# Kernel tuning notes

Hardware: AMD Instinct MI355X
Metric: run time of the kernel (lower is better)

The kernel has to match this reference:

```python
import jax, jax.numpy as jnp
import numpy as np

N_NODES = 20000
N_EDGES = 320000
N_GRAPHS = 64
D = 128  # node_dim


def _gat_conv(h, W, al, ar, b, src, dst, n, res=None, act=None):
    # DGL GATConv: fc -> per-head attn logits -> leaky_relu -> edge softmax per dst -> scatter-add
    H, Dh = al.shape
    feat = (h @ W).reshape(n, H, Dh)                      # [N,H,D]
    el = jnp.einsum('nhd,hd->nh', feat, al)               # [N,H]
    er = jnp.einsum('nhd,hd->nh', feat, ar)               # [N,H]
    e = jax.nn.leaky_relu(el[src] + er[dst], 0.2)         # [E,H]
    m = jax.ops.segment_max(e, dst, num_segments=n)       # [N,H]
    m = jnp.where(jnp.isfinite(m), m, 0.0)
    a = jnp.exp(e - m[dst])                               # [E,H]
    den = jax.ops.segment_sum(a, dst, num_segments=n)     # [N,H]
    a = a / jnp.maximum(den, 1e-9)[dst]
    out = jax.ops.segment_sum(a[:, :, None] * feat[src], dst, num_segments=n)  # [N,H,D]
    if res is not None:
        out = out + res
    out = out + b.reshape(1, H, Dh)
    return act(out) if act is not None else out


def setup_inputs() -> dict:
    key = jax.random.key(0)
    ks = jax.random.split(key, 20)
    s = 0.05
    inp = {
        'h': jax.random.normal(ks[0], (N_NODES, D), jnp.float32),
        'he': jax.random.normal(ks[1], (N_EDGES, 64), jnp.float32),
        'src': jax.random.randint(ks[2], (N_EDGES,), 0, N_NODES),
        'dst': jax.random.randint(ks[3], (N_EDGES,), 0, N_NODES),
        'graph_id': jnp.sort(jax.random.randint(ks[4], (N_NODES,), 0, N_GRAPHS)),
        # layer 0: in=D, heads=4, out=D
        'W0': jax.random.normal(ks[5], (D, 4 * D), jnp.float32) * s,
        'al0': jax.random.normal(ks[6], (4, D), jnp.float32) * s,
        'ar0': jax.random.normal(ks[7], (4, D), jnp.float32) * s,
        'b0': jnp.zeros((4 * D,), jnp.float32),
        # layer 1: in=4D, heads=4, out=D, residual (identity since 4D==4*D)
        'W1': jax.random.normal(ks[8], (4 * D, 4 * D), jnp.float32) * s,
        'al1': jax.random.normal(ks[9], (4, D), jnp.float32) * s,
        'ar1': jax.random.normal(ks[10], (4, D), jnp.float32) * s,
        'b1': jnp.zeros((4 * D,), jnp.float32),
        # layer 2: in=4D, heads=6, out=D, residual via res_fc (4D -> 6D)
        'W2': jax.random.normal(ks[11], (4 * D, 6 * D), jnp.float32) * s,
        'al2': jax.random.normal(ks[12], (6, D), jnp.float32) * s,
        'ar2': jax.random.normal(ks[13], (6, D), jnp.float32) * s,
        'b2': jnp.zeros((6 * D,), jnp.float32),
        'resW2': jax.random.normal(ks[14], (4 * D, 6 * D), jnp.float32) * s,
        # final MLP (1 layer): Linear(D, D)
        'Wm': jax.random.normal(ks[15], (D, D), jnp.float32) * s,
        'bm': jnp.zeros((D,), jnp.float32),
    }
    return inp


def reference(h, he, src, dst, graph_id, W0, al0, ar0, b0, W1, al1, ar1, b1,
              W2, al2, ar2, b2, resW2, Wm, bm):
    n = h.shape[0]
    elu = jax.nn.elu
    # layer 0 (no residual, elu), flatten heads
    x = _gat_conv(h, W0, al0, ar0, b0, src, dst, n, res=None, act=elu)
    x = x.reshape(n, -1)  # [N, 4D]
    # layer 1 (identity residual, elu), flatten heads
    res1 = x.reshape(n, 4, D)
    x2 = _gat_conv(x, W1, al1, ar1, b1, src, dst, n, res=res1, act=elu)
    x2 = x2.reshape(n, -1)  # [N, 4D]
    # layer 2 (linear residual, no activation), mean over heads
    res2 = (x2 @ resW2).reshape(n, 6, D)
    x3 = _gat_conv(x2, W2, al2, ar2, b2, src, dst, n, res=res2, act=None)
    local_feat = x3.mean(axis=1)  # [N, D]
    # avg pooling per graph + linear
    sums = jax.ops.segment_sum(local_feat, graph_id, num_segments=N_GRAPHS)
    cnts = jax.ops.segment_sum(jnp.ones((n,), local_feat.dtype), graph_id, num_segments=N_GRAPHS)
    pooled = sums / jnp.maximum(cnts, 1.0)[:, None]  # [G, D]
    global_feat = pooled @ Wm + bm
    return (local_feat, global_feat)
```

## Files before the change

### kernel.cpp

```cpp
#include <hip/hip_runtime.h>
#include <math.h>


typedef _Float16 f16;
typedef __attribute__((ext_vector_type(8))) _Float16 half8;
typedef __attribute__((ext_vector_type(4))) _Float16 half4;
typedef __attribute__((ext_vector_type(4))) float float4v;

union U16 { unsigned short u; _Float16 h; };

#define M_PAD 20096
#define CHSTRIDE ((size_t)M_PAD * 64)

__device__ inline void gload_lds16(const void* g, void* l) {
    __builtin_amdgcn_global_load_lds((const __attribute__((address_space(1))) unsigned*)g,
                                     (__attribute__((address_space(3))) unsigned*)l,
                                     16, 0, 0);
}


__global__ __launch_bounds__(256) void deg_kernel(const int* __restrict__ dst,
                                                  int* __restrict__ deg, int E) {
    int e = blockIdx.x * 256 + threadIdx.x;
    if (e < E) atomicAdd(&deg[dst[e]], 1);
}

__global__ __launch_bounds__(1024) void scan_kernel(const int* __restrict__ deg,
                                                    int* __restrict__ row_off,
                                                    const int* __restrict__ gid,
                                                    int* __restrict__ gstart, int n) {
    __shared__ int sums[1024];
    int t = threadIdx.x;
    if (t <= 64) {
        int g = t, lo = 0, hi = n;
        while (lo < hi) {
            int mid = (lo + hi) >> 1;
            if (gid[mid] < g) lo = mid + 1; else hi = mid;
        }
        gstart[g] = lo;
    }
    int CH = (n + 1023) >> 10;
    int base = t * CH;
    int s = 0;
    for (int i = 0; i < CH; ++i) { int idx = base + i; if (idx < n) s += deg[idx]; }
    sums[t] = s;
    __syncthreads();
    for (int off = 1; off < 1024; off <<= 1) {
        int v = (t >= off) ? sums[t - off] : 0;
        __syncthreads();
        sums[t] += v;
        __syncthreads();
    }
    int run = (t == 0) ? 0 : sums[t - 1];
    for (int i = 0; i < CH; ++i) {
        int idx = base + i;
        if (idx < n) { row_off[idx] = run; run += deg[idx]; }
    }
    if (t == 1023) row_off[n] = run;
}

__global__ __launch_bounds__(256) void fill_kernel(const int* __restrict__ src,
                                                   const int* __restrict__ dst,
                                                   const int* __restrict__ row_off,
                                                   int* __restrict__ fill,
                                                   int* __restrict__ csr_src, int E) {
    int e = blockIdx.x * 256 + threadIdx.x;
    if (e < E) {
        int d = dst[e];
        int pos = row_off[d] + atomicAdd(&fill[d], 1);
        csr_src[pos] = src[e];
    }
}


__global__ __launch_bounds__(256) void cvt_pad_kernel(const float* __restrict__ x,
                                                      f16* __restrict__ y,
                                                      long n_valid, long n_total) {
    long i = ((long)blockIdx.x * 256 + threadIdx.x) * 4;
    if (i >= n_total) return;
    float4 v = make_float4(0.f, 0.f, 0.f, 0.f);
    if (i < n_valid) v = *(const float4*)&x[i];
    half4 o; o[0] = (f16)v.x; o[1] = (f16)v.y; o[2] = (f16)v.z; o[3] = (f16)v.w;
    *(half4*)&y[i] = o;
}

__global__ __launch_bounds__(256) void zero_pad_kernel(f16* __restrict__ x1,
                                                       f16* __restrict__ x2, int n) {
    int total = (M_PAD - n) * 512;
    int idx = (blockIdx.x * 256 + threadIdx.x) * 4;
    if (idx < total) {
        half4 z; z[0] = (f16)0.f; z[1] = (f16)0.f; z[2] = (f16)0.f; z[3] = (f16)0.f;
        *(half4*)&x1[(size_t)n * 512 + idx] = z;
        *(half4*)&x2[(size_t)n * 512 + idx] = z;
    }
}

__global__ __launch_bounds__(256) void transpose_cvt_kernel(const float* __restrict__ W,
                                                            f16* __restrict__ Wt,
                                                            int K, int N) {
    __shared__ float tile[32][33];
    int n0 = blockIdx.x * 32, k0 = blockIdx.y * 32;
    int tx = threadIdx.x, ty = threadIdx.y;
#pragma unroll
    for (int i = 0; i < 32; i += 8)
        tile[ty + i][tx] = W[(size_t)(k0 + ty + i) * N + n0 + tx];
    __syncthreads();
#pragma unroll
    for (int i = 0; i < 32; i += 8)
        Wt[(size_t)(n0 + ty + i) * K + k0 + tx] = (f16)tile[tx][ty + i];
}


__global__ __launch_bounds__(256) void gemm16_kernel(const f16* __restrict__ A,
                                                     const f16* __restrict__ Bt,
                                                     f16* __restrict__ Cc,
                                                     f16* __restrict__ Cr,
                                                     const float* __restrict__ al,
                                                     const float* __restrict__ ar,
                                                     float* __restrict__ el8,
                                                     float* __restrict__ er8,
                                                     int N, int K, int nchunk,
                                                     int nheads, int nvalid) {
    __shared__ f16 As[128 * 32];
    __shared__ f16 Bs[128 * 32];
    __shared__ float elds[2][2][128];
    int t = threadIdx.x;
    int w = t >> 6;
    int l = t & 63;
    size_t bm = (size_t)blockIdx.y * 128;
    int bn = blockIdx.x * 128;
    int wm = (w & 1) * 64;
    int wn = (w >> 1) * 64;

    int srow = t >> 2;
    int sq = (t & 3) ^ ((srow >> 1) & 3);
    const f16* ag0 = A + (bm + srow) * K + sq * 8;
    const f16* ag1 = A + (bm + 64 + srow) * K + sq * 8;
    const f16* bg0 = Bt + (size_t)(bn + srow) * K + sq * 8;
    const f16* bg1 = Bt + (size_t)(bn + 64 + srow) * K + sq * 8;
    f16* al0 = As + t * 8;
    f16* al1 = As + 2048 + t * 8;
    f16* bl0 = Bs + t * 8;
    f16* bl1 = Bs + 2048 + t * 8;

    float4v acc[4][4];
#pragma unroll
    for (int i = 0; i < 4; ++i)
#pragma unroll
        for (int j = 0; j < 4; ++j) acc[i][j] = (float4v)(0.f);

    int ml = l & 15, q = l >> 4;
    int sslot = (q ^ ((ml >> 1) & 3)) * 8;
    const f16* ap = As + (wm + ml) * 32 + sslot;
    const f16* bp = Bs + (wn + ml) * 32 + sslot;

    for (int k0 = 0; k0 < K; k0 += 32) {
        gload_lds16(ag0 + k0, al0);
        gload_lds16(ag1 + k0, al1);
        gload_lds16(bg0 + k0, bl0);
        gload_lds16(bg1 + k0, bl1);
        __syncthreads();
        half8 af[4], bf[4];
#pragma unroll
        for (int mt = 0; mt < 4; ++mt) af[mt] = *(const half8*)(ap + mt * 16 * 32);
#pragma unroll
        for (int nt = 0; nt < 4; ++nt) bf[nt] = *(const half8*)(bp + nt * 16 * 32);
#pragma unroll
        for (int mt = 0; mt < 4; ++mt)
#pragma unroll
            for (int nt = 0; nt < 4; ++nt)
                acc[mt][nt] = __builtin_amdgcn_mfma_f32_16x16x32_f16(bf[nt], af[mt],
                                                                     acc[mt][nt], 0, 0, 0);
        __syncthreads();
    }
#pragma unroll
    for (int mt = 0; mt < 4; ++mt) {
        size_t row = bm + wm + mt * 16 + ml;
#pragma unroll
        for (int nt = 0; nt < 4; ++nt) {
            half4 hv;
#pragma unroll
            for (int r = 0; r < 4; ++r) hv[r] = (f16)acc[mt][nt][r];
            int col = bn + wn + nt * 16 + q * 4;
            if (col < nchunk) {
                *(half4*)&Cc[(size_t)(col >> 6) * CHSTRIDE + row * 64 + (col & 63)] = hv;
            } else {
                *(half4*)&Cr[row * (size_t)(N - nchunk) + (col - nchunk)] = hv;
            }
        }
    }
    if (al != nullptr && bn < nheads * 128) {
        int hh = bn >> 7;
        float4 a4[4], r4[4];
#pragma unroll
        for (int nt = 0; nt < 4; ++nt) {
            int ci = hh * 128 + wn + nt * 16 + q * 4;
            a4[nt] = *(const float4*)&al[ci];
            r4[nt] = *(const float4*)&ar[ci];
        }
        int wnidx = wn >> 6;
#pragma unroll
        for (int mt = 0; mt < 4; ++mt) {
            float ep = 0.f, rp = 0.f;
#pragma unroll
            for (int nt = 0; nt < 4; ++nt) {
                ep += acc[mt][nt][0] * a4[nt].x + acc[mt][nt][1] * a4[nt].y
                    + acc[mt][nt][2] * a4[nt].z + acc[mt][nt][3] * a4[nt].w;
                rp += acc[mt][nt][0] * r4[nt].x + acc[mt][nt][1] * r4[nt].y
                    + acc[mt][nt][2] * r4[nt].z + acc[mt][nt][3] * r4[nt].w;
            }
            ep += __shfl_xor(ep, 16, 64); ep += __shfl_xor(ep, 32, 64);
            rp += __shfl_xor(rp, 16, 64); rp += __shfl_xor(rp, 32, 64);
            if (q == 0) {
                elds[0][wnidx][wm + mt * 16 + ml] = ep;
                elds[1][wnidx][wm + mt * 16 + ml] = rp;
            }
        }
        __syncthreads();
        int row = t & 127, which = t >> 7;
        long gv = (long)bm + row;
        if (gv < nvalid) {
            float vs = elds[which][0][row] + elds[which][1][row];
            if (which == 0) el8[gv * 8 + hh] = vs;
            else            er8[gv * 8 + hh] = vs;
        }
    }
}


__global__ __launch_bounds__(256, 8) void edge_weight_kernel(
        const float* __restrict__ el8, const float* __restrict__ er8,
        const int* __restrict__ row_off, const int* __restrict__ csr_src,
        unsigned short* __restrict__ wexp, float* __restrict__ inv8,
        int H, int n, int E) {
    int wid = threadIdx.x >> 6, lane = threadIdx.x & 63;
    int c2 = lane >> 4;
    int sl = lane & 15;
    int v = blockIdx.x * 16 + wid * 4 + c2;
    if (v >= n) return;
    float era[6];
    {
        float4 a = *(const float4*)&er8[(size_t)v * 8];
        float2 b = *(const float2*)&er8[(size_t)v * 8 + 4];
        era[0] = a.x; era[1] = a.y; era[2] = a.z; era[3] = a.w;
        era[4] = b.x; era[5] = b.y;
    }
    int beg = row_off[v], end = row_off[v + 1];
    float lsum[6] = {0.f, 0.f, 0.f, 0.f, 0.f, 0.f};
    for (int pos = beg; pos < end; pos += 16) {
        int cnt = min(16, end - pos);
        int s_l = (sl < cnt) ? csr_src[pos + sl] : 0;
        float4 a = *(const float4*)&el8[(size_t)s_l * 8];
        float2 bq = *(const float2*)&el8[(size_t)s_l * 8 + 4];
        float ee[6] = {a.x, a.y, a.z, a.w, bq.x, bq.y};
#pragma unroll
        for (int h = 0; h < 6; ++h) {
            if (h < H) {
                float lg = ee[h] + era[h];
                lg = (lg >= 0.f) ? lg : 0.2f * lg;
                float wv = __expf(lg);
                if (sl >= cnt) wv = 0.f;
                lsum[h] += wv;
                if (sl < cnt) {
                    U16 uu; uu.h = (f16)wv;
                    wexp[(size_t)h * E + pos + sl] = uu.u;
                }
            }
        }
    }
#pragma unroll
    for (int h = 0; h < 6; ++h)
#pragma unroll
        for (int off = 8; off >= 1; off >>= 1)
            lsum[h] += __shfl_xor(lsum[h], off, 64);
    if (sl == 0) {
#pragma unroll
        for (int h = 0; h < 6; ++h)
            if (h < H) inv8[(size_t)v * 8 + h] = 1.f / fmaxf(lsum[h], 1e-9f);
    }
}


__device__ __forceinline__ void agg_chunk_body(
        const f16* __restrict__ fc, const unsigned short* __restrict__ wh,
        const float* __restrict__ inv8, int head,
        const int* __restrict__ row_off, const int* __restrict__ csr_src,
        const f16* __restrict__ res, const float* __restrict__ bias,
        f16* __restrict__ out16, float* __restrict__ out32,
        int n, int width, int act, int chunk,
        int wave_id, int wavestride, int lane) {
    int c = lane >> 3;
    int j = lane & 7;
    int coff = j * 8;
    int cb = chunk * 64 + coff;
    float4 bv0 = *(const float4*)&bias[cb];
    float4 bv1 = *(const float4*)&bias[cb + 4];
    int clbase = lane & 56;

    for (int v0 = wave_id * 8; v0 < n; v0 += wavestride * 8) {
        int v = v0 + c;
        bool valid = (v < n);
        int beg = 0, end = 0;
        if (valid) { beg = row_off[v]; end = row_off[v + 1]; }
        int rounds = end - beg;
        rounds = max(rounds, __shfl_xor(rounds, 8, 64));
        rounds = max(rounds, __shfl_xor(rounds, 16, 64));
        rounds = max(rounds, __shfl_xor(rounds, 32, 64));
        float acc[8] = {0.f, 0.f, 0.f, 0.f, 0.f, 0.f, 0.f, 0.f};
        int s_pf = 0, w_pf = 0;
        for (int r = 0; r < rounds; ++r) {
            if ((r & 7) == 0) {
                int pidx = beg + r + j;
                bool ok = pidx < end;
                s_pf = ok ? csr_src[pidx] : 0;
                w_pf = ok ? (int)wh[pidx] : 0;
            }
            int srcl = clbase + (r & 7);
            int s  = __shfl(s_pf, srcl, 64);
            int wi = __shfl(w_pf, srcl, 64);
            U16 uu; uu.u = (unsigned short)wi;
            float wv = (float)uu.h;
            half8 f = *(const half8*)&fc[(size_t)s * 64 + coff];
#pragma unroll
            for (int k = 0; k < 8; ++k) acc[k] += wv * (float)f[k];
        }
        if (valid) {
            float inv = inv8[(size_t)v * 8 + head];
            float ox[8];
#pragma unroll
            for (int k = 0; k < 8; ++k) ox[k] = acc[k] * inv;
            size_t base = (size_t)v * width + cb;
            if (res) {
                half8 rr = *(const half8*)&res[base];
#pragma unroll
                for (int k = 0; k < 8; ++k) ox[k] += (float)rr[k];
            }
            ox[0] += bv0.x; ox[1] += bv0.y; ox[2] += bv0.z; ox[3] += bv0.w;
            ox[4] += bv1.x; ox[5] += bv1.y; ox[6] += bv1.z; ox[7] += bv1.w;
            if (act) {
#pragma unroll
                for (int k = 0; k < 8; ++k)
                    ox[k] = (ox[k] > 0.f) ? ox[k] : expm1f(ox[k]);
            }
            if (out16) {
                half8 o;
#pragma unroll
                for (int k = 0; k < 8; ++k) o[k] = (f16)ox[k];
                *(half8*)&out16[base] = o;
            } else {
                *(float4*)&out32[base]     = make_float4(ox[0], ox[1], ox[2], ox[3]);
                *(float4*)&out32[base + 4] = make_float4(ox[4], ox[5], ox[6], ox[7]);
            }
        }
    }
}

__global__ __launch_bounds__(256, 8) void agg_chunk_kernel(
        const f16* __restrict__ featc, const unsigned short* __restrict__ wexp,
        const float* __restrict__ inv8,
        const int* __restrict__ row_off, const int* __restrict__ csr_src,
        const f16* __restrict__ res, const float* __restrict__ bias,
        f16* __restrict__ out16, float* __restrict__ out32,
        int n, int nchunks, int width, int E, int act) {
    int wid = threadIdx.x >> 6, lane = threadIdx.x & 63;
    int b = blockIdx.x;
    {
        int chunk = b & 7;
        agg_chunk_body(featc + (size_t)chunk * CHSTRIDE, wexp + (size_t)(chunk >> 1) * E,
                       inv8, chunk >> 1, row_off, csr_src, res, bias, out16, out32,
                       n, width, act, chunk, (b >> 3) * 4 + wid, 1024, lane);
    }
    if (nchunks > 8) {
        int chunk = 8 + (b & 3);
        if (chunk < nchunks)
            agg_chunk_body(featc + (size_t)chunk * CHSTRIDE, wexp + (size_t)(chunk >> 1) * E,
                           inv8, chunk >> 1, row_off, csr_src, res, bias, out16, out32,
                           n, width, act, chunk, (b >> 2) * 4 + wid, 2048, lane);
    }
}


__global__ __launch_bounds__(128) void mean_pool_kernel(const float* __restrict__ x3,
                                                        float* __restrict__ local, int n) {
    int v = blockIdx.x;
    int d = threadIdx.x;
    const float* p = x3 + (size_t)v * 768;
    float s = 0.f;
#pragma unroll
    for (int h = 0; h < 6; ++h) s += p[h * 128 + d];
    local[(size_t)v * 128 + d] = s * (1.f / 6.f);
}

__global__ __launch_bounds__(256) void graph_pool_kernel(const float* __restrict__ local,
                                                         const int* __restrict__ gstart,
                                                         float* __restrict__ pooled) {
    __shared__ float buf[128];
    int g = blockIdx.x;
    int t = threadIdx.x;
    int c = t & 127;
    int sub = t >> 7;
    int beg = gstart[g], end = gstart[g + 1];
    float s = 0.f;
    for (int v = beg + sub; v < end; v += 2) s += local[(size_t)v * 128 + c];
    if (sub == 1) buf[c] = s;
    __syncthreads();
    if (sub == 0) {
        float tot = s + buf[c];
        float cntf = fmaxf((float)(end - beg), 1.f);
        pooled[g * 128 + c] = tot / cntf;
    }
}

__global__ void final_mlp_kernel(const float* __restrict__ pooled,
                                 const float* __restrict__ Wm,
                                 const float* __restrict__ bm,
                                 float* __restrict__ gout) {
    int g = blockIdx.x;
    int j = threadIdx.x;
    __shared__ float p[128];
    p[j] = pooled[g * 128 + j];
    __syncthreads();
    float s = 0.f;
#pragma unroll 16
    for (int k = 0; k < 128; ++k) s += p[k] * Wm[k * 128 + j];
    gout[g * 128 + j] = s + bm[j];
}


extern "C" void kernel_launch(void* const* d_in, const int* in_sizes, int n_in,
                              void* d_out, int out_size, void* d_ws, size_t ws_size,
                              hipStream_t stream) {
    const float* h     = (const float*)d_in[0];
    const int*   src   = (const int*)d_in[2];
    const int*   dst   = (const int*)d_in[3];
    const int*   gid   = (const int*)d_in[4];
    const float* W0    = (const float*)d_in[5];
    const float* al0   = (const float*)d_in[6];
    const float* ar0   = (const float*)d_in[7];
    const float* b0    = (const float*)d_in[8];
    const float* W1    = (const float*)d_in[9];
    const float* al1   = (const float*)d_in[10];
    const float* ar1   = (const float*)d_in[11];
    const float* b1    = (const float*)d_in[12];
    const float* W2    = (const float*)d_in[13];
    const float* al2   = (const float*)d_in[14];
    const float* ar2   = (const float*)d_in[15];
    const float* b2    = (const float*)d_in[16];
    const float* resW2 = (const float*)d_in[17];
    const float* Wm    = (const float*)d_in[18];
    const float* bm    = (const float*)d_in[19];

    const int n = in_sizes[0] / 128;
    const int E = in_sizes[2];

    size_t off = 0;
    auto take = [&](size_t bytes) -> void* {
        void* p = (char*)d_ws + off;
        off = (off + bytes + 255) & ~(size_t)255;
        return p;
    };
    f16* h16     = (f16*)take((size_t)M_PAD * 128 * 2);
    f16* Wt0     = (f16*)take((size_t)512 * 128 * 2);
    f16* Wt1     = (f16*)take((size_t)512 * 512 * 2);
    f16* Wt2cat  = (f16*)take((size_t)1536 * 512 * 2);
    f16* featc   = (f16*)take((size_t)12 * CHSTRIDE * 2);
    f16* res2    = (f16*)take((size_t)M_PAD * 768 * 2);
    f16* x1_16   = (f16*)take((size_t)M_PAD * 512 * 2);
    f16* x2_16   = (f16*)take((size_t)M_PAD * 512 * 2);
    float* x3    = (float*)take((size_t)n * 768 * 4);
    unsigned short* wexp = (unsigned short*)take((size_t)6 * E * 2);
    float* inv8  = (float*)take((size_t)n * 8 * 4);
    float* el8   = (float*)take((size_t)n * 8 * 4);
    float* er8   = (float*)take((size_t)n * 8 * 4);
    int* deg     = (int*)take((size_t)2 * n * 4);
    int* fillc   = deg + n;
    int* row_off = (int*)take((size_t)(n + 1) * 4);
    int* csr_src = (int*)take((size_t)E * 4);
    int* gstart  = (int*)take(65 * 4);
    float* pooled = (float*)take(64 * 128 * 4);

    float* out_local  = (float*)d_out;
    float* out_global = (float*)d_out + (size_t)n * 128;

    hipMemsetAsync(deg, 0, (size_t)2 * n * 4, stream);
    zero_pad_kernel<<<(int)(((size_t)(M_PAD - n) * 512 / 4 + 255) / 256), 256, 0, stream>>>(x1_16, x2_16, n);

    {
        long nv = (long)n * 128, nt = (long)M_PAD * 128;
        cvt_pad_kernel<<<(int)((nt / 4 + 255) / 256), 256, 0, stream>>>(h, h16, nv, nt);
    }
    transpose_cvt_kernel<<<dim3(512 / 32, 128 / 32), dim3(32, 8), 0, stream>>>(W0, Wt0, 128, 512);
    transpose_cvt_kernel<<<dim3(512 / 32, 512 / 32), dim3(32, 8), 0, stream>>>(W1, Wt1, 512, 512);
    transpose_cvt_kernel<<<dim3(768 / 32, 512 / 32), dim3(32, 8), 0, stream>>>(W2, Wt2cat, 512, 768);
    transpose_cvt_kernel<<<dim3(768 / 32, 512 / 32), dim3(32, 8), 0, stream>>>(resW2, Wt2cat + (size_t)768 * 512, 512, 768);

    deg_kernel<<<(E + 255) / 256, 256, 0, stream>>>(dst, deg, E);
    scan_kernel<<<1, 1024, 0, stream>>>(deg, row_off, gid, gstart, n);
    fill_kernel<<<(E + 255) / 256, 256, 0, stream>>>(src, dst, row_off, fillc, csr_src, E);

    const int gy = M_PAD / 128;
    const int ew_blocks = (n + 15) / 16;

    gemm16_kernel<<<dim3(512 / 128, gy), 256, 0, stream>>>(h16, Wt0, featc, nullptr,
                                                           al0, ar0, el8, er8, 512, 128, 512, 4, n);
    edge_weight_kernel<<<ew_blocks, 256, 0, stream>>>(el8, er8, row_off, csr_src, wexp, inv8, 4, n, E);
    agg_chunk_kernel<<<2048, 256, 0, stream>>>(featc, wexp, inv8, row_off, csr_src,
                                               nullptr, b0, x1_16, nullptr, n, 8, 512, E, 1);
    gemm16_kernel<<<dim3(512 / 128, gy), 256, 0, stream>>>(x1_16, Wt1, featc, nullptr,
                                                           al1, ar1, el8, er8, 512, 512, 512, 4, n);
    edge_weight_kernel<<<ew_blocks, 256, 0, stream>>>(el8, er8, row_off, csr_src, wexp, inv8, 4, n, E);
    agg_chunk_kernel<<<2048, 256, 0, stream>>>(featc, wexp, inv8, row_off, csr_src,
                                               x1_16, b1, x2_16, nullptr, n, 8, 512, E, 1);
    gemm16_kernel<<<dim3(1536 / 128, gy), 256, 0, stream>>>(x2_16, Wt2cat, featc, res2,
                                                            al2, ar2, el8, er8, 1536, 512, 768, 6, n);
    edge_weight_kernel<<<ew_blocks, 256, 0, stream>>>(el8, er8, row_off, csr_src, wexp, inv8, 6, n, E);
    agg_chunk_kernel<<<2048, 256, 0, stream>>>(featc, wexp, inv8, row_off, csr_src,
                                               res2, b2, nullptr, x3, n, 12, 768, E, 0);
    mean_pool_kernel<<<n, 128, 0, stream>>>(x3, out_local, n);
    graph_pool_kernel<<<64, 256, 0, stream>>>(out_local, gstart, pooled);
    final_mlp_kernel<<<64, 128, 0, stream>>>(pooled, Wm, bm, out_global);
}
```

Baseline: 569.2 us.

## Double-buffer GEMM LDS tiles and swizzle workgroups across XCDs

The fp16 MFMA GEMM now uses two LDS buffers and issues the next K-tile's global-to-LDS loads before computing on the current tile, so load latency can overlap with MFMA work instead of stalling behind a barrier each iteration. Workgroup IDs are also remapped so that consecutive tiles land on the same XCD, which is meant to improve L2 reuse of shared A/B rows. The cost is double the LDS per block, which may lower occupancy. Relying on a single barrier per iteration with async LDS loads also risks a race unless the loads are correctly waited on.

```diff
diff --git a/kernel.cpp b/kernel.cpp
--- a/kernel.cpp
+++ b/kernel.cpp
@@ -111,6 +111,15 @@
 }
 
 
+#define STAGE(buf, k0) do {                                   \
+    f16* a_ = As + (buf) * 4096 + t * 8;                      \
+    f16* b_ = Bs + (buf) * 4096 + t * 8;                      \
+    gload_lds16(ag0 + (k0), a_);                              \
+    gload_lds16(ag1 + (k0), a_ + 2048);                       \
+    gload_lds16(bg0 + (k0), b_);                              \
+    gload_lds16(bg1 + (k0), b_ + 2048);                       \
+} while (0)
+
 __global__ __launch_bounds__(256) void gemm16_kernel(const f16* __restrict__ A,
                                                      const f16* __restrict__ Bt,
                                                      f16* __restrict__ Cc,
@@ -121,14 +130,24 @@
                                                      float* __restrict__ er8,
                                                      int N, int K, int nchunk,
                                                      int nheads, int nvalid) {
-    __shared__ f16 As[128 * 32];
-    __shared__ f16 Bs[128 * 32];
+    __shared__ f16 As[2 * 128 * 32];
+    __shared__ f16 Bs[2 * 128 * 32];
     __shared__ float elds[2][2][128];
     int t = threadIdx.x;
     int w = t >> 6;
     int l = t & 63;
-    size_t bm = (size_t)blockIdx.y * 128;
-    int bn = blockIdx.x * 128;
+
+    int gx = gridDim.x;
+    int nwg = gx * gridDim.y;
+    int wg = blockIdx.y * gx + blockIdx.x;
+    int qq = nwg >> 3, rr = nwg & 7;
+    int xcd = wg & 7, idx = wg >> 3;
+    int swz = (xcd < rr ? xcd * (qq + 1) : rr * (qq + 1) + (xcd - rr) * qq) + idx;
+    int bxi = swz % gx;
+    int byi = swz / gx;
+
+    size_t bm = (size_t)byi * 128;
+    int bn = bxi * 128;
     int wm = (w & 1) * 64;
     int wn = (w >> 1) * 64;
 
@@ -138,10 +157,6 @@
     const f16* ag1 = A + (bm + 64 + srow) * K + sq * 8;
     const f16* bg0 = Bt + (size_t)(bn + srow) * K + sq * 8;
     const f16* bg1 = Bt + (size_t)(bn + 64 + srow) * K + sq * 8;
-    f16* al0 = As + t * 8;
-    f16* al1 = As + 2048 + t * 8;
-    f16* bl0 = Bs + t * 8;
-    f16* bl1 = Bs + 2048 + t * 8;
 
     float4v acc[4][4];
 #pragma unroll
@@ -151,15 +166,16 @@
 
     int ml = l & 15, q = l >> 4;
     int sslot = (q ^ ((ml >> 1) & 3)) * 8;
-    const f16* ap = As + (wm + ml) * 32 + sslot;
-    const f16* bp = Bs + (wn + ml) * 32 + sslot;
-
+    int apoff = (wm + ml) * 32 + sslot;
+    int bpoff = (wn + ml) * 32 + sslot;
+
+    STAGE(0, 0);
+    __syncthreads();
+    int cur = 0;
     for (int k0 = 0; k0 < K; k0 += 32) {
-        gload_lds16(ag0 + k0, al0);
-        gload_lds16(ag1 + k0, al1);
-        gload_lds16(bg0 + k0, bl0);
-        gload_lds16(bg1 + k0, bl1);
-        __syncthreads();
+        if (k0 + 32 < K) STAGE(cur ^ 1, k0 + 32);
+        const f16* ap = As + cur * 4096 + apoff;
+        const f16* bp = Bs + cur * 4096 + bpoff;
         half8 af[4], bf[4];
 #pragma unroll
         for (int mt = 0; mt < 4; ++mt) af[mt] = *(const half8*)(ap + mt * 16 * 32);
@@ -172,6 +188,7 @@
                 acc[mt][nt] = __builtin_amdgcn_mfma_f32_16x16x32_f16(bf[nt], af[mt],
                                                                      acc[mt][nt], 0, 0, 0);
         __syncthreads();
+        cur ^= 1;
     }
 #pragma unroll
     for (int mt = 0; mt < 4; ++mt) {
```

After: 555.5 us. 1.02x faster.
